# Optimization experiments

Hardware: AMD Instinct MI355X
Metric: run time of the kernel (lower is better)

Reference implementation:

```python
import jax, jax.numpy as jnp
import numpy as np

BN_EPS = 1e-5


def _lin(x, W, b):
    return x @ W.T + b


def reference(input, first_skeleton, noise, first_W, first_b, gru_Wih, gru_Whh,
              gru_bih, gru_bhh, l0_W, l0_b, res_W, res_b, bn_g, bn_b, bn_m, bn_v,
              fl1_W, fl1_b, fl2_W, fl2_b, fl3_W, fl3_b, qkv_W,
              posm_W1, posm_b1, posm_W2, posm_b2, attn_W1, attn_b1, attn_W2, attn_b2):
    B = input.shape[0]
    # first skeleton embedding -> (B, 50, 1)
    sk = _lin(first_skeleton.reshape(B, 36), first_W, first_b).reshape(B, 50, 1)
    # GRU(10 -> 10), batch_first, h0 = 0
    def gru_step(h, x_t):
        gi = x_t @ gru_Wih.T + gru_bih          # (B, 30)
        gh = h @ gru_Whh.T + gru_bhh
        ir, iz, i_n = jnp.split(gi, 3, axis=-1)
        hr, hz, h_n = jnp.split(gh, 3, axis=-1)
        r = jax.nn.sigmoid(ir + hr)
        z = jax.nn.sigmoid(iz + hz)
        n = jnp.tanh(i_n + r * h_n)
        h_new = (1.0 - z) * n + z * h
        return h_new, h_new
    h0 = jnp.zeros((B, 10), input.dtype)
    _, aux = jax.lax.scan(gru_step, h0, jnp.swapaxes(noise, 0, 1))  # (50, B, 10)
    aux = jnp.tanh(jnp.swapaxes(aux, 0, 1))                          # (B, 50, 10)
    x = jnp.concatenate([input, aux, sk], axis=2).reshape(-1, 267)   # (B*50, 267)
    out = _lin(x, l0_W, l0_b)                                        # (B*50, 1024)
    # three residual Linear+BN(eval)+ReLU blocks
    for i in range(3):
        y = out
        for j in range(2):
            y = _lin(y, res_W[i, j], res_b[i, j])
            y = bn_g[i, j] * (y - bn_m[i, j]) * jax.lax.rsqrt(bn_v[i, j] + BN_EPS) + bn_b[i, j]
            y = jax.nn.relu(y)
        out = y + out
    # dropout: eval mode (identity)
    feats = _lin(out, fl1_W, fl1_b).reshape(B, 50, 128)
    pos = _lin(out, fl2_W, fl2_b).reshape(B, 50, 3)
    # PointTransformerLayer (full attention, mask all True -> no-op)
    qkv = feats @ qkv_W.T                                   # (B, 50, 384)
    q, k, v = jnp.split(qkv, 3, axis=-1)
    rel_pos = pos[:, :, None, :] - pos[:, None, :, :]        # (B, 50, 50, 3)
    rel_emb = _lin(jax.nn.relu(_lin(rel_pos, posm_W1, posm_b1)), posm_W2, posm_b2)  # (B,50,50,128)
    qk_rel = q[:, :, None, :] - k[:, None, :, :]             # (B, 50, 50, 128)
    v_ij = v[:, None, :, :] + rel_emb                        # (B, 50, 50, 128)
    sim = _lin(jax.nn.relu(_lin(qk_rel + rel_emb, attn_W1, attn_b1)), attn_W2, attn_b2)
    attn = jax.nn.softmax(sim, axis=-2)                      # softmax over j
    agg = jnp.einsum('bijd,bijd->bid', attn, v_ij)           # (B, 50, 128)
    o = jnp.tanh(_lin(agg, fl3_W, fl3_b))                    # (B, 50, 36)
    return o


def setup_inputs() -> dict:
    key = jax.random.key(0)
    ks = iter(jax.random.split(key, 64))
    def W(*s):
        return jax.random.normal(next(ks), s, jnp.float32) * 0.02
    B = 256
    z = lambda *s: jnp.zeros(s, jnp.float32)
    return {
        'input': jax.random.normal(next(ks), (B, 50, 256), jnp.float32),
        'first_skeleton': jax.random.normal(next(ks), (B, 36), jnp.float32),
        'noise': jax.random.normal(next(ks), (B, 50, 10), jnp.float32) * 0.33,
        'first_W': W(50, 36), 'first_b': z(50),
        'gru_Wih': W(30, 10), 'gru_Whh': W(30, 10), 'gru_bih': z(30), 'gru_bhh': z(30),
        'l0_W': W(1024, 267), 'l0_b': z(1024),
        'res_W': W(3, 2, 1024, 1024), 'res_b': z(3, 2, 1024),
        'bn_g': jnp.ones((3, 2, 1024), jnp.float32), 'bn_b': z(3, 2, 1024),
        'bn_m': z(3, 2, 1024), 'bn_v': jnp.ones((3, 2, 1024), jnp.float32),
        'fl1_W': W(128, 1024), 'fl1_b': z(128),
        'fl2_W': W(3, 1024), 'fl2_b': z(3),
        'fl3_W': W(36, 128), 'fl3_b': z(36),
        'qkv_W': W(384, 128),
        'posm_W1': W(64, 3), 'posm_b1': z(64), 'posm_W2': W(128, 64), 'posm_b2': z(128),
        'attn_W1': W(512, 128), 'attn_b1': z(512), 'attn_W2': W(128, 512), 'attn_b2': z(128),
    }
```

## Files before the change

kernel.cpp:

```cpp
#include <hip/hip_runtime.h>

typedef __attribute__((ext_vector_type(8))) short bf16x8;
typedef __attribute__((ext_vector_type(4))) float f32x4;
typedef __attribute__((ext_vector_type(4))) ushort u16x4;

__device__ __forceinline__ unsigned f2b2(float lo, float hi) {
    unsigned r;
    asm("v_cvt_pk_bf16_f32 %0, %1, %2" : "=v"(r) : "v"(lo), "v"(hi));
    return r;
}
__device__ __forceinline__ ushort f2b(float v) {
    return (ushort)f2b2(v, v);
}
__device__ __forceinline__ float b2f(ushort b) {
    union { float f; unsigned u; } x; x.u = ((unsigned)b) << 16; return x.f;
}

__device__ __forceinline__ void gl_lds16(const void* g, void* l) {
    __builtin_amdgcn_global_load_lds(
        (__attribute__((address_space(1))) void*)(g),
        (__attribute__((address_space(3))) void*)(l), 16, 0, 0);
}


__global__ void k_split(const float* __restrict__ src, ushort* __restrict__ hi,
                        ushort* __restrict__ lo, int rows, int K, int Kpad) {
    long total = (long)rows * Kpad;
    for (long idx = (long)blockIdx.x * 256 + threadIdx.x; idx < total;
         idx += (long)gridDim.x * 256) {
        int r = (int)(idx / Kpad), c = (int)(idx % Kpad);
        float v = (c < K) ? src[(long)r * K + c] : 0.f;
        ushort h = f2b(v);
        hi[idx] = h;
        if (lo) lo[idx] = f2b(v - b2f(h));
    }
}

__global__ void k_wc(const float* __restrict__ qkvW, const float* __restrict__ fl1W,
                     const float* __restrict__ fl1b, float* __restrict__ Wc,
                     float* __restrict__ bc) {
    int idx = blockIdx.x * 256 + threadIdx.x;
    if (idx >= 384 * 1024) return;
    int n = idx >> 10, k = idx & 1023;
    float s = 0.f;
    #pragma unroll 8
    for (int d = 0; d < 128; ++d) s += qkvW[n * 128 + d] * fl1W[d * 1024 + k];
    Wc[idx] = s;
    if (k == 0) {
        float sb = 0.f;
        #pragma unroll 8
        for (int d = 0; d < 128; ++d) sb += qkvW[n * 128 + d] * fl1b[d];
        bc[n] = sb;
    }
}

__global__ void k_sk(const float* __restrict__ fs, const float* __restrict__ fW,
                     const float* __restrict__ fb, float* __restrict__ sk) {
    int m = blockIdx.x * 256 + threadIdx.x;
    if (m >= 12800) return;
    int b = m / 50, i = m % 50;
    float s = fb[i];
    #pragma unroll 4
    for (int c = 0; c < 36; ++c) s += fs[b * 36 + c] * fW[i * 36 + c];
    sk[m] = s;
}

__global__ void k_gru(const float* __restrict__ noise, const float* __restrict__ Wih,
                      const float* __restrict__ Whh, const float* __restrict__ bih,
                      const float* __restrict__ bhh, float* __restrict__ aux) {
    int lane = threadIdx.x & 63;
    int b = blockIdx.x;
    if (b >= 256) return;
    float wih[10] = {}, whh[10] = {};
    float bi = 0.f, bh = 0.f;
    if (lane < 30) {
        #pragma unroll
        for (int c = 0; c < 10; ++c) { wih[c] = Wih[lane * 10 + c]; whh[c] = Whh[lane * 10 + c]; }
        bi = bih[lane]; bh = bhh[lane];
    }
    float h = 0.f;
    for (int t = 0; t < 50; ++t) {
        float xr = (lane < 10) ? noise[(b * 50 + t) * 10 + lane] : 0.f;
        float gi = bi, gh = bh;
        #pragma unroll
        for (int c = 0; c < 10; ++c) {
            float xc = __shfl(xr, c, 64);
            float hc = __shfl(h, c, 64);
            gi += wih[c] * xc; gh += whh[c] * hc;
        }
        float siz = __shfl(gi, lane + 10, 64), shz = __shfl(gh, lane + 10, 64);
        float sin_ = __shfl(gi, lane + 20, 64), shn = __shfl(gh, lane + 20, 64);
        float r = 1.f / (1.f + expf(-(gi + gh)));
        float z = 1.f / (1.f + expf(-(siz + shz)));
        float n = tanhf(sin_ + r * shn);
        float hn = (1.f - z) * n + z * h;
        if (lane < 10) { h = hn; aux[(b * 50 + t) * 10 + lane] = tanhf(hn); }
    }
}

__global__ void k_xbuild(const float* __restrict__ input, const float* __restrict__ aux,
                         const float* __restrict__ sk, ushort* __restrict__ xhi,
                         long M) {
    long idx = (long)blockIdx.x * 256 + threadIdx.x;
    if (idx >= M * 288) return;
    int m = (int)(idx / 288), c = (int)(idx % 288);
    float v;
    if (c < 256) v = input[(long)m * 256 + c];
    else if (c < 266) v = aux[m * 10 + (c - 256)];
    else if (c == 266) v = sk[m];
    else v = 0.f;
    xhi[idx] = f2b(v);
}

template <int MODE>
__global__ __launch_bounds__(256, 3) void k_gemm(
    const ushort* __restrict__ Ahi,
    const ushort* __restrict__ Bhi,
    int N, int K,
    float* outF, ushort* outHi,
    const float* __restrict__ bias,
    const float* __restrict__ bng, const float* __restrict__ bnb,
    const float* __restrict__ bnm, const float* __restrict__ bnv,
    const ushort* resHi) {
    __shared__ __align__(16) ushort S[2][128][32];
    int t = threadIdx.x;
    int flat = blockIdx.y * gridDim.x + blockIdx.x;
    int nwg = gridDim.x * gridDim.y;
    int q = nwg >> 3, r = nwg & 7;
    int xcd = flat & 7, seq = flat >> 3;
    int wgid = (xcd < r ? xcd * (q + 1) : r * (q + 1) + (xcd - r) * q) + seq;
    int bx = wgid % gridDim.x, by = wgid / gridDim.x;
    int m0 = by * 128, n0 = bx * 128;
    int w = t >> 6, lane = t & 63;
    int wm = w >> 1, wn = w & 1;
    int lo16 = lane & 15, hi4 = lane >> 4;

    const int srow = lane >> 2;
    const int skoff = ((lane & 3) ^ (srow & 3)) * 8;
    const int slot8 = (hi4 ^ (lo16 & 3)) * 8;

    f32x4 acc[4][4];
    #pragma unroll
    for (int i = 0; i < 4; ++i)
        #pragma unroll
        for (int j = 0; j < 4; ++j) acc[i][j] = f32x4{0.f, 0.f, 0.f, 0.f};

    const int nk = K / 32;
    for (int kt = 0; kt < nk; ++kt) {
        const int kb = kt * 32;
        #pragma unroll
        for (int i = 0; i < 2; ++i) {
            int rg = w * 32 + i * 16;
            long ga = (long)(m0 + rg + srow) * K + kb + skoff;
            long gb = (long)(n0 + rg + srow) * K + kb + skoff;
            gl_lds16(&Ahi[ga], &S[0][rg][0]);
            gl_lds16(&Bhi[gb], &S[1][rg][0]);
        }
        __syncthreads();
        bf16x8 ah[4], bh[4];
        #pragma unroll
        for (int m = 0; m < 4; ++m) {
            int row = wm * 64 + m * 16 + lo16;
            ah[m] = *(const bf16x8*)&S[0][row][slot8];
        }
        #pragma unroll
        for (int n = 0; n < 4; ++n) {
            int col = wn * 64 + n * 16 + lo16;
            bh[n] = *(const bf16x8*)&S[1][col][slot8];
        }
        #pragma unroll
        for (int m = 0; m < 4; ++m)
            #pragma unroll
            for (int n = 0; n < 4; ++n)
                acc[m][n] = __builtin_amdgcn_mfma_f32_16x16x32_bf16(ah[m], bh[n], acc[m][n], 0, 0, 0);
        __syncthreads();
    }

    #pragma unroll
    for (int n = 0; n < 4; ++n) {
        int gn = n0 + wn * 64 + n * 16 + lo16;
        float bv = bias ? bias[gn] : 0.f;
        float sc = 1.f, sh = 0.f;
        if (MODE >= 1) { sc = bng[gn] * rsqrtf(bnv[gn] + 1e-5f); sh = bnb[gn] - bnm[gn] * sc; }
        #pragma unroll
        for (int m = 0; m < 4; ++m)
            #pragma unroll
            for (int r2 = 0; r2 < 4; ++r2) {
                int gm = m0 + wm * 64 + m * 16 + hi4 * 4 + r2;
                long o = (long)gm * N + gn;
                float v = acc[m][n][r2] + bv;
                if (MODE >= 1) v = fmaxf(v * sc + sh, 0.f);
                if (MODE == 2) v += b2f(resHi[o]);
                if (outF) outF[o] = v;
                if (outHi) outHi[o] = f2b(v);
            }
    }
}

__global__ void k_fl2(const ushort* __restrict__ hA,
                      const float* __restrict__ W, const float* __restrict__ bias,
                      float* __restrict__ pos) {
    int w = threadIdx.x >> 6, lane = threadIdx.x & 63;
    int m = blockIdx.x * 4 + w;
    float a0 = 0.f, a1 = 0.f, a2 = 0.f;
    for (int k0 = lane * 4; k0 < 1024; k0 += 256) {
        long o = (long)m * 1024 + k0;
        u16x4 hv = *(const u16x4*)&hA[o];
        f32x4 w0 = *(const f32x4*)&W[k0];
        f32x4 w1 = *(const f32x4*)&W[1024 + k0];
        f32x4 w2 = *(const f32x4*)&W[2048 + k0];
        #pragma unroll
        for (int e = 0; e < 4; ++e) {
            float x = b2f(hv[e]);
            a0 += x * w0[e]; a1 += x * w1[e]; a2 += x * w2[e];
        }
    }
    #pragma unroll
    for (int off = 32; off; off >>= 1) {
        a0 += __shfl_xor(a0, off, 64);
        a1 += __shfl_xor(a1, off, 64);
        a2 += __shfl_xor(a2, off, 64);
    }
    if (lane == 0) {
        pos[m * 3 + 0] = a0 + bias[0];
        pos[m * 3 + 1] = a1 + bias[1];
        pos[m * 3 + 2] = a2 + bias[2];
    }
}

__global__ __launch_bounds__(256, 3) void k_attn2(
    const float* __restrict__ qkv, const float* __restrict__ posb,
    const ushort* __restrict__ W1b, const ushort* __restrict__ W2b,
    const float* __restrict__ b1, const ushort* __restrict__ pW2b,
    const float* __restrict__ pW1, const float* __restrict__ pb1,
    const float* __restrict__ pb2,
    const float* __restrict__ fl3W, const float* __restrict__ fl3b,
    float* __restrict__ out, long mbase) {
    __shared__ __align__(16) char smem[49152];
    int flat = blockIdx.x, nwg = gridDim.x;
    int q = nwg >> 3, r = nwg & 7;
    int xcd = flat & 7, seq = flat >> 3;
    int wgid = (xcd < r ? xcd * (q + 1) : r * (q + 1) + (xcd - r) * q) + seq;
    int bi0 = wgid * 2;
    int t = threadIdx.x, w = t >> 6, lane = t & 63;
    int lo16 = lane & 15, hi4 = lane >> 4;
    char* H1 = smem + 32768;

    {
        int rl = t & 127, eh = t >> 7;
        int biL = bi0 + (rl >> 6);
        int j = rl & 63; int jc = j < 50 ? j : 49;
        int bL = biL / 50;
        int kv = bL * 50 + jc;
        float d0 = posb[biL * 3] - posb[kv * 3];
        float d1 = posb[biL * 3 + 1] - posb[kv * 3 + 1];
        float d2 = posb[biL * 3 + 2] - posb[kv * 3 + 2];
        int swm = (rl & 7) << 4;
        #pragma unroll
        for (int e0 = 0; e0 < 32; e0 += 2) {
            int e = eh * 32 + e0;
            float v0 = fmaxf(pb1[e] + pW1[e * 3] * d0 + pW1[e * 3 + 1] * d1
                             + pW1[e * 3 + 2] * d2, 0.f);
            float v1 = fmaxf(pb1[e + 1] + pW1[e * 3 + 3] * d0 + pW1[e * 3 + 4] * d1
                             + pW1[e * 3 + 5] * d2, 0.f);
            *(unsigned*)(H1 + rl * 128 + ((e * 2) ^ swm)) = f2b2(v0, v1);
        }
    }
    __syncthreads();

    {
        f32x4 racc[8][2];
        #pragma unroll
        for (int m = 0; m < 8; ++m)
            #pragma unroll
            for (int n = 0; n < 2; ++n) racc[m][n] = f32x4{0.f, 0.f, 0.f, 0.f};
        #pragma unroll
        for (int kt = 0; kt < 2; ++kt) {
            int k0 = kt * 32 + hi4 * 8;
            bf16x8 bv[2];
            #pragma unroll
            for (int n = 0; n < 2; ++n)
                bv[n] = *(const bf16x8*)&pW2b[(w * 32 + n * 16 + lo16) * 64 + k0];
            #pragma unroll
            for (int m = 0; m < 8; ++m) {
                int row = m * 16 + lo16;
                bf16x8 ha = *(const bf16x8*)(H1 + row * 128 + ((k0 * 2) ^ ((lo16 & 7) << 4)));
                #pragma unroll
                for (int n = 0; n < 2; ++n)
                    racc[m][n] = __builtin_amdgcn_mfma_f32_16x16x32_bf16(ha, bv[n], racc[m][n], 0, 0, 0);
            }
        }
        #pragma unroll
        for (int m = 0; m < 8; ++m)
            #pragma unroll
            for (int n = 0; n < 2; ++n) {
                int col = w * 32 + n * 16 + lo16;
                float pb = pb2[col];
                #pragma unroll
                for (int rr = 0; rr < 4; ++rr) {
                    int row = m * 16 + hi4 * 4 + rr;
                    *(ushort*)(smem + row * 256 + ((col * 2) ^ ((row & 15) << 4))) =
                        f2b(racc[m][n][rr] + pb);
                }
            }
    }
    __syncthreads();

    #pragma unroll
    for (int cc = 0; cc < 8; ++cc) {
        int c = cc * 256 + t;
        int row = c >> 4, g16 = c & 15;
        int biL = bi0 + (row >> 6);
        int j = row & 63;
        char* addr = smem + row * 256 + ((g16 * 16) ^ ((row & 15) << 4));
        bf16x8 tv;
        if (j < 50) {
            int bL = biL / 50;
            long kq = (long)biL * 384 + g16 * 8;
            long kk = (long)(bL * 50 + j) * 384 + 128 + g16 * 8;
            f32x4 q0 = *(const f32x4*)&qkv[kq];
            f32x4 q1 = *(const f32x4*)&qkv[kq + 4];
            f32x4 k0v = *(const f32x4*)&qkv[kk];
            f32x4 k1v = *(const f32x4*)&qkv[kk + 4];
            bf16x8 rv = *(bf16x8*)addr;
            unsigned* tu = (unsigned*)&tv;
            #pragma unroll
            for (int i = 0; i < 2; ++i)
                tu[i] = f2b2(q0[2 * i] - k0v[2 * i] + b2f((ushort)rv[2 * i]),
                             q0[2 * i + 1] - k0v[2 * i + 1] + b2f((ushort)rv[2 * i + 1]));
            #pragma unroll
            for (int i = 0; i < 2; ++i)
                tu[2 + i] = f2b2(q1[2 * i] - k1v[2 * i] + b2f((ushort)rv[4 + 2 * i]),
                                 q1[2 * i + 1] - k1v[2 * i + 1] + b2f((ushort)rv[4 + 2 * i + 1]));
        } else {
            #pragma unroll
            for (int e = 0; e < 8; ++e) tv[e] = 0;
        }
        *(bf16x8*)addr = tv;
    }
    __syncthreads();

    f32x4 acc2[8][2];
    #pragma unroll
    for (int m = 0; m < 8; ++m)
        #pragma unroll
        for (int n = 0; n < 2; ++n) acc2[m][n] = f32x4{0.f, 0.f, 0.f, 0.f};

    for (int e8 = 0; e8 < 8; ++e8) {
        f32x4 acc1[8];
        #pragma unroll
        for (int m = 0; m < 8; ++m) acc1[m] = f32x4{0.f, 0.f, 0.f, 0.f};
        __builtin_amdgcn_s_setprio(1);
        #pragma unroll
        for (int kt = 0; kt < 4; ++kt) {
            int col = e8 * 64 + w * 16 + lo16;
            int k0 = kt * 32 + hi4 * 8;
            bf16x8 bfv = *(const bf16x8*)&W1b[(long)col * 128 + k0];
            #pragma unroll
            for (int m = 0; m < 8; ++m) {
                int row = m * 16 + lo16;
                bf16x8 af = *(const bf16x8*)(smem + row * 256 +
                              ((k0 * 2) ^ ((row & 15) << 4)));
                acc1[m] = __builtin_amdgcn_mfma_f32_16x16x32_bf16(af, bfv, acc1[m], 0, 0, 0);
            }
        }
        __builtin_amdgcn_s_setprio(0);
        __syncthreads();
        {
            int ch = w * 16 + lo16;
            float bb = b1[e8 * 64 + ch];
            #pragma unroll
            for (int m = 0; m < 8; ++m) {
                unsigned p01 = f2b2(fmaxf(acc1[m][0] + bb, 0.f), fmaxf(acc1[m][1] + bb, 0.f));
                unsigned p23 = f2b2(fmaxf(acc1[m][2] + bb, 0.f), fmaxf(acc1[m][3] + bb, 0.f));
                int r0 = m * 16 + hi4 * 4;
                *(ushort*)(H1 + (r0 + 0) * 128 + ((ch * 2) ^ (((r0 + 0) & 7) << 4))) = (ushort)p01;
                *(ushort*)(H1 + (r0 + 1) * 128 + ((ch * 2) ^ (((r0 + 1) & 7) << 4))) = (ushort)(p01 >> 16);
                *(ushort*)(H1 + (r0 + 2) * 128 + ((ch * 2) ^ (((r0 + 2) & 7) << 4))) = (ushort)p23;
                *(ushort*)(H1 + (r0 + 3) * 128 + ((ch * 2) ^ (((r0 + 3) & 7) << 4))) = (ushort)(p23 >> 16);
            }
        }
        __syncthreads();
        #pragma unroll
        for (int kt2 = 0; kt2 < 2; ++kt2) {
            int k0 = kt2 * 32 + hi4 * 8;
            bf16x8 af2[8];
            #pragma unroll
            for (int m = 0; m < 8; ++m) {
                int row = m * 16 + lo16;
                af2[m] = *(const bf16x8*)(H1 + row * 128 + ((k0 * 2) ^ ((lo16 & 7) << 4)));
            }
            __builtin_amdgcn_s_setprio(1);
            #pragma unroll
            for (int n = 0; n < 2; ++n) {
                int col = w * 32 + n * 16 + lo16;
                bf16x8 w2 = *(const bf16x8*)&W2b[(long)col * 512 + e8 * 64 + k0];
                #pragma unroll
                for (int m = 0; m < 8; ++m)
                    acc2[m][n] = __builtin_amdgcn_mfma_f32_16x16x32_bf16(af2[m], w2, acc2[m][n], 0, 0, 0);
            }
            __builtin_amdgcn_s_setprio(0);
        }
    }
    __syncthreads();

    {
        int rl = t & 127, eh = t >> 7;
        int biL = bi0 + (rl >> 6);
        int j = rl & 63; int jc = j < 50 ? j : 49;
        int bL = biL / 50;
        int kv = bL * 50 + jc;
        float d0 = posb[biL * 3] - posb[kv * 3];
        float d1 = posb[biL * 3 + 1] - posb[kv * 3 + 1];
        float d2 = posb[biL * 3 + 2] - posb[kv * 3 + 2];
        int swm = (rl & 7) << 4;
        #pragma unroll
        for (int e0 = 0; e0 < 32; e0 += 2) {
            int e = eh * 32 + e0;
            float v0 = fmaxf(pb1[e] + pW1[e * 3] * d0 + pW1[e * 3 + 1] * d1
                             + pW1[e * 3 + 2] * d2, 0.f);
            float v1 = fmaxf(pb1[e + 1] + pW1[e * 3 + 3] * d0 + pW1[e * 3 + 4] * d1
                             + pW1[e * 3 + 5] * d2, 0.f);
            *(unsigned*)(H1 + rl * 128 + ((e * 2) ^ swm)) = f2b2(v0, v1);
        }
    }
    __syncthreads();

    #pragma unroll 1
    for (int mh = 0; mh < 2; ++mh) {
        f32x4 racc[4][2];
        #pragma unroll
        for (int m = 0; m < 4; ++m)
            #pragma unroll
            for (int n = 0; n < 2; ++n) racc[m][n] = f32x4{0.f, 0.f, 0.f, 0.f};
        #pragma unroll
        for (int kt = 0; kt < 2; ++kt) {
            int k0 = kt * 32 + hi4 * 8;
            bf16x8 bv[2];
            #pragma unroll
            for (int n = 0; n < 2; ++n)
                bv[n] = *(const bf16x8*)&pW2b[(w * 32 + n * 16 + lo16) * 64 + k0];
            #pragma unroll
            for (int m = 0; m < 4; ++m) {
                int row = (mh * 4 + m) * 16 + lo16;
                bf16x8 ha = *(const bf16x8*)(H1 + row * 128 + ((k0 * 2) ^ ((lo16 & 7) << 4)));
                #pragma unroll
                for (int n = 0; n < 2; ++n)
                    racc[m][n] = __builtin_amdgcn_mfma_f32_16x16x32_bf16(ha, bv[n], racc[m][n], 0, 0, 0);
            }
        }
        #pragma unroll
        for (int m = 0; m < 4; ++m)
            #pragma unroll
            for (int n = 0; n < 2; ++n) {
                int col = w * 32 + n * 16 + lo16;
                float pb = pb2[col];
                #pragma unroll
                for (int rr = 0; rr < 4; ++rr) {
                    int row = (mh * 4 + m) * 16 + hi4 * 4 + rr;
                    *(ushort*)(smem + row * 256 + ((col * 2) ^ ((row & 15) << 4))) =
                        f2b(racc[m][n][rr] + pb);
                }
            }
    }
    __syncthreads();

    float* aggF = (float*)H1;
    float* part = (float*)(H1 + 1024);
    #pragma unroll
    for (int bs = 0; bs < 2; ++bs) {
        int biL = bi0 + bs;
        int bL = biL / 50;
        float outv[2];
        #pragma unroll
        for (int n = 0; n < 2; ++n) {
            float mx = -1e30f;
            #pragma unroll
            for (int m = 0; m < 4; ++m)
                #pragma unroll
                for (int rr = 0; rr < 4; ++rr) {
                    int j = m * 16 + hi4 * 4 + rr;
                    if (j < 50) mx = fmaxf(mx, acc2[bs * 4 + m][n][rr]);
                }
            mx = fmaxf(mx, __shfl_xor(mx, 16, 64));
            mx = fmaxf(mx, __shfl_xor(mx, 32, 64));
            float e[4][4];
            float sum = 0.f;
            #pragma unroll
            for (int m = 0; m < 4; ++m)
                #pragma unroll
                for (int rr = 0; rr < 4; ++rr) {
                    int j = m * 16 + hi4 * 4 + rr;
                    float ev = (j < 50) ? __expf(acc2[bs * 4 + m][n][rr] - mx) : 0.f;
                    e[m][rr] = ev; sum += ev;
                }
            sum += __shfl_xor(sum, 16, 64);
            sum += __shfl_xor(sum, 32, 64);
            float inv = 1.f / sum;
            int col = w * 32 + n * 16 + lo16;
            float ag = 0.f;
            #pragma unroll
            for (int m = 0; m < 4; ++m)
                #pragma unroll
                for (int rr = 0; rr < 4; ++rr) {
                    int j = m * 16 + hi4 * 4 + rr;
                    if (j < 50) {
                        int row = bs * 64 + j;
                        float rl = b2f(*(const ushort*)(smem + row * 256 +
                                      ((col * 2) ^ ((j & 15) << 4))));
                        float vv = qkv[(long)(bL * 50 + j) * 384 + 256 + col] + rl;
                        ag += e[m][rr] * inv * vv;
                    }
                }
            ag += __shfl_xor(ag, 16, 64);
            ag += __shfl_xor(ag, 32, 64);
            outv[n] = ag;
        }
        if (hi4 == 0) {
            aggF[bs * 128 + w * 32 + lo16] = outv[0];
            aggF[bs * 128 + w * 32 + 16 + lo16] = outv[1];
        }
        if (lane < 36) {
            const float* wf = &fl3W[lane * 128 + w * 32];
            const float* af = aggF + bs * 128 + w * 32;
            float s = 0.f;
            #pragma unroll 8
            for (int d = 0; d < 32; ++d) s += af[d] * wf[d];
            part[bs * 144 + w * 36 + lane] = s;
        }
    }
    __syncthreads();

    if (t < 36) {
        float s = fl3b[t] + part[t] + part[36 + t] + part[72 + t] + part[108 + t];
        out[(mbase + bi0) * 36 + t] = tanhf(s);
    } else if (t >= 128 && t < 164) {
        int tt = t - 128;
        float s = fl3b[tt] + part[144 + tt] + part[144 + 36 + tt]
                + part[144 + 72 + tt] + part[144 + 108 + tt];
        out[(mbase + bi0 + 1) * 36 + tt] = tanhf(s);
    }
}

struct Bufs {
    float *sk, *aux, *qkvF, *posb, *WcF, *bc;
    ushort *xh, *actAh, *actBh;
    ushort *l0Wh, *resWh, *Wch, *aW1b, *aW2b, *pW2b;
};

static size_t plan_ws(char* ws, long MCr, Bufs& B) {
    size_t off = 0;
    auto alloc = [&](size_t n) { char* p = ws + off; off += (n + 255) & ~(size_t)255; return p; };
    B.sk    = (float*) alloc(12800L * 4);
    B.aux   = (float*) alloc(128000L * 4);
    B.xh    = (ushort*)alloc((size_t)MCr * 288 * 2);
    B.actAh = (ushort*)alloc((size_t)MCr * 1024 * 2);
    B.actBh = (ushort*)alloc((size_t)MCr * 1024 * 2);
    B.qkvF  = (float*) alloc((size_t)MCr * 384 * 4);
    B.posb  = (float*) alloc((size_t)MCr * 3 * 4);
    B.l0Wh  = (ushort*)alloc(1024L * 288 * 2);
    B.resWh = (ushort*)alloc(6144L * 1024 * 2);
    B.WcF   = (float*) alloc(384L * 1024 * 4);
    B.Wch   = (ushort*)alloc(384L * 1024 * 2);
    B.bc    = (float*) alloc(384L * 4);
    B.aW1b  = (ushort*)alloc(512L * 128 * 2);
    B.aW2b  = (ushort*)alloc(128L * 512 * 2);
    B.pW2b  = (ushort*)alloc(128L * 64 * 2);
    return off;
}

extern "C" void kernel_launch(void* const* d_in, const int* in_sizes, int n_in,
                              void* d_out, int out_size, void* d_ws, size_t ws_size,
                              hipStream_t stream) {
    (void)in_sizes; (void)n_in;
    const float* input  = (const float*)d_in[0];
    const float* fskel  = (const float*)d_in[1];
    const float* noise  = (const float*)d_in[2];
    const float* firstW = (const float*)d_in[3];
    const float* firstB = (const float*)d_in[4];
    const float* gWih   = (const float*)d_in[5];
    const float* gWhh   = (const float*)d_in[6];
    const float* gbih   = (const float*)d_in[7];
    const float* gbhh   = (const float*)d_in[8];
    const float* l0W    = (const float*)d_in[9];
    const float* l0b    = (const float*)d_in[10];
    const float* resW   = (const float*)d_in[11];
    const float* resB   = (const float*)d_in[12];
    const float* bnG    = (const float*)d_in[13];
    const float* bnB    = (const float*)d_in[14];
    const float* bnM    = (const float*)d_in[15];
    const float* bnV    = (const float*)d_in[16];
    const float* fl1W   = (const float*)d_in[17];
    const float* fl1b   = (const float*)d_in[18];
    const float* fl2W   = (const float*)d_in[19];
    const float* fl2b   = (const float*)d_in[20];
    const float* fl3W   = (const float*)d_in[21];
    const float* fl3b   = (const float*)d_in[22];
    const float* qkvW   = (const float*)d_in[23];
    const float* pW1    = (const float*)d_in[24];
    const float* pb1    = (const float*)d_in[25];
    const float* pW2    = (const float*)d_in[26];
    const float* pb2    = (const float*)d_in[27];
    const float* aW1    = (const float*)d_in[28];
    const float* ab1    = (const float*)d_in[29];
    const float* aW2    = (const float*)d_in[30];
    float* out = (float*)d_out;

    char* ws = (char*)d_ws;
    Bufs B;
    long MCr = 12800;
    while (plan_ws(ws, MCr, B) > ws_size) {
        MCr >>= 1;
        if (MCr < 1600) {
            hipMemsetAsync(d_out, 0, (size_t)out_size * sizeof(float), stream);
            return;
        }
    }
    const int nchunks = (int)(12800 / MCr);

    k_split<<<1152, 256, 0, stream>>>(l0W, B.l0Wh, nullptr, 1024, 267, 288);
    k_split<<<8192, 256, 0, stream>>>(resW, B.resWh, nullptr, 6144, 1024, 1024);
    k_wc<<<1536, 256, 0, stream>>>(qkvW, fl1W, fl1b, B.WcF, B.bc);
    k_split<<<1536, 256, 0, stream>>>(B.WcF, B.Wch, nullptr, 384, 1024, 1024);
    k_split<<<256, 256, 0, stream>>>(aW1, B.aW1b, nullptr, 512, 128, 128);
    k_split<<<256, 256, 0, stream>>>(aW2, B.aW2b, nullptr, 128, 512, 512);
    k_split<<<32, 256, 0, stream>>>(pW2, B.pW2b, nullptr, 128, 64, 64);
    k_sk<<<50, 256, 0, stream>>>(fskel, firstW, firstB, B.sk);
    k_gru<<<256, 64, 0, stream>>>(noise, gWih, gWhh, gbih, gbhh, B.aux);

    for (int c = 0; c < nchunks; ++c) {
        long mbase = (long)c * MCr;
        int xb_grid = (int)((MCr * 288 + 255) / 256);
        k_xbuild<<<xb_grid, 256, 0, stream>>>(input + mbase * 256, B.aux + mbase * 10,
                                              B.sk + mbase, B.xh, MCr);
        dim3 gt(8, (unsigned)(MCr / 128));
        k_gemm<0><<<gt, 256, 0, stream>>>(B.xh, B.l0Wh, 1024, 288,
            nullptr, B.actAh, l0b, nullptr, nullptr, nullptr, nullptr, nullptr);
        for (int blk = 0; blk < 3; ++blk) {
            int j0 = blk * 2, j1 = blk * 2 + 1;
            k_gemm<1><<<gt, 256, 0, stream>>>(B.actAh,
                B.resWh + (size_t)j0 * 1024 * 1024,
                1024, 1024, nullptr, B.actBh, resB + j0 * 1024,
                bnG + j0 * 1024, bnB + j0 * 1024, bnM + j0 * 1024, bnV + j0 * 1024,
                nullptr);
            k_gemm<2><<<gt, 256, 0, stream>>>(B.actBh,
                B.resWh + (size_t)j1 * 1024 * 1024,
                1024, 1024, nullptr, B.actAh, resB + j1 * 1024,
                bnG + j1 * 1024, bnB + j1 * 1024, bnM + j1 * 1024, bnV + j1 * 1024,
                B.actAh);
        }
        dim3 gq(3, (unsigned)(MCr / 128));
        k_gemm<0><<<gq, 256, 0, stream>>>(B.actAh, B.Wch, 384, 1024,
            B.qkvF, nullptr, B.bc, nullptr, nullptr, nullptr, nullptr, nullptr);
        k_fl2<<<(int)(MCr / 4), 256, 0, stream>>>(B.actAh, fl2W, fl2b, B.posb);
        k_attn2<<<(int)(MCr / 2), 256, 0, stream>>>(B.qkvF, B.posb, B.aW1b, B.aW2b,
                                                    ab1, B.pW2b, pW1, pb1, pb2,
                                                    fl3W, fl3b, out, mbase);
    }
}
```

Before: 1.063 ms.

## Process attention rows one at a time, spilling second row's logits to LDS in fp16

The second query row's attention logits (acc2[4..7]) are packed to fp16 and parked in shared memory. The rel-pos embedding and softmax/aggregation then run in a loop over the two rows, one at a time. This roughly halves the live accumulator registers in the epilogue and the LDS footprint for the rel-pos MLP, which could allow more occupancy. In exchange it adds an extra barrier per row, serialises the two rows, and reduces the second row's logits to fp16 precision.

```diff
diff --git a/kernel.cpp b/kernel.cpp
--- a/kernel.cpp
+++ b/kernel.cpp
@@ -14,6 +14,14 @@
 }
 __device__ __forceinline__ float b2f(ushort b) {
     union { float f; unsigned u; } x; x.u = ((unsigned)b) << 16; return x.f;
+}
+__device__ __forceinline__ unsigned pkf16(float a, float b) {
+    unsigned r;
+    asm("v_cvt_pkrtz_f16_f32 %0, %1, %2" : "=v"(r) : "v"(a), "v"(b));
+    return r;
+}
+__device__ __forceinline__ float h2f(ushort s) {
+    union { ushort s; _Float16 h; } x; x.s = s; return (float)x.h;
 }
 
 __device__ __forceinline__ void gl_lds16(const void* g, void* l) {
@@ -405,72 +413,101 @@
     __syncthreads();
 
     {
-        int rl = t & 127, eh = t >> 7;
-        int biL = bi0 + (rl >> 6);
-        int j = rl & 63; int jc = j < 50 ? j : 49;
-        int bL = biL / 50;
-        int kv = bL * 50 + jc;
-        float d0 = posb[biL * 3] - posb[kv * 3];
-        float d1 = posb[biL * 3 + 1] - posb[kv * 3 + 1];
-        float d2 = posb[biL * 3 + 2] - posb[kv * 3 + 2];
-        int swm = (rl & 7) << 4;
-        #pragma unroll
-        for (int e0 = 0; e0 < 32; e0 += 2) {
-            int e = eh * 32 + e0;
-            float v0 = fmaxf(pb1[e] + pW1[e * 3] * d0 + pW1[e * 3 + 1] * d1
-                             + pW1[e * 3 + 2] * d2, 0.f);
-            float v1 = fmaxf(pb1[e + 1] + pW1[e * 3 + 3] * d0 + pW1[e * 3 + 4] * d1
-                             + pW1[e * 3 + 5] * d2, 0.f);
-            *(unsigned*)(H1 + rl * 128 + ((e * 2) ^ swm)) = f2b2(v0, v1);
-        }
-    }
-    __syncthreads();
+        unsigned* P = (unsigned*)H1;
+        #pragma unroll
+        for (int m = 0; m < 4; ++m)
+            #pragma unroll
+            for (int n = 0; n < 2; ++n) {
+                P[((m * 2 + n) * 2 + 0) * 256 + t] = pkf16(acc2[4 + m][n][0], acc2[4 + m][n][1]);
+                P[((m * 2 + n) * 2 + 1) * 256 + t] = pkf16(acc2[4 + m][n][2], acc2[4 + m][n][3]);
+            }
+    }
+
+    float* aggF = (float*)(smem + 24576);
+    float* part = (float*)(smem + 25088);
 
     #pragma unroll 1
-    for (int mh = 0; mh < 2; ++mh) {
-        f32x4 racc[4][2];
-        #pragma unroll
-        for (int m = 0; m < 4; ++m)
-            #pragma unroll
-            for (int n = 0; n < 2; ++n) racc[m][n] = f32x4{0.f, 0.f, 0.f, 0.f};
-        #pragma unroll
-        for (int kt = 0; kt < 2; ++kt) {
-            int k0 = kt * 32 + hi4 * 8;
-            bf16x8 bv[2];
-            #pragma unroll
-            for (int n = 0; n < 2; ++n)
-                bv[n] = *(const bf16x8*)&pW2b[(w * 32 + n * 16 + lo16) * 64 + k0];
-            #pragma unroll
-            for (int m = 0; m < 4; ++m) {
-                int row = (mh * 4 + m) * 16 + lo16;
-                bf16x8 ha = *(const bf16x8*)(H1 + row * 128 + ((k0 * 2) ^ ((lo16 & 7) << 4)));
-                #pragma unroll
-                for (int n = 0; n < 2; ++n)
-                    racc[m][n] = __builtin_amdgcn_mfma_f32_16x16x32_bf16(ha, bv[n], racc[m][n], 0, 0, 0);
-            }
-        }
-        #pragma unroll
-        for (int m = 0; m < 4; ++m)
-            #pragma unroll
-            for (int n = 0; n < 2; ++n) {
-                int col = w * 32 + n * 16 + lo16;
-                float pb = pb2[col];
-                #pragma unroll
-                for (int rr = 0; rr < 4; ++rr) {
-                    int row = (mh * 4 + m) * 16 + hi4 * 4 + rr;
-                    *(ushort*)(smem + row * 256 + ((col * 2) ^ ((row & 15) << 4))) =
-                        f2b(racc[m][n][rr] + pb);
-                }
-            }
-    }
-    __syncthreads();
-
-    float* aggF = (float*)H1;
-    float* part = (float*)(H1 + 1024);
-    #pragma unroll
     for (int bs = 0; bs < 2; ++bs) {
         int biL = bi0 + bs;
         int bL = biL / 50;
+        f32x4 cur[4][2];
+        if (bs == 0) {
+            #pragma unroll
+            for (int m = 0; m < 4; ++m)
+                #pragma unroll
+                for (int n = 0; n < 2; ++n) cur[m][n] = acc2[m][n];
+        } else {
+            const unsigned* P = (const unsigned*)H1;
+            #pragma unroll
+            for (int m = 0; m < 4; ++m)
+                #pragma unroll
+                for (int n = 0; n < 2; ++n) {
+                    unsigned u0 = P[((m * 2 + n) * 2 + 0) * 256 + t];
+                    unsigned u1 = P[((m * 2 + n) * 2 + 1) * 256 + t];
+                    cur[m][n][0] = h2f((ushort)u0);
+                    cur[m][n][1] = h2f((ushort)(u0 >> 16));
+                    cur[m][n][2] = h2f((ushort)u1);
+                    cur[m][n][3] = h2f((ushort)(u1 >> 16));
+                }
+        }
+        {
+            int rl = t & 63, eq = t >> 6;
+            int jc = rl < 50 ? rl : 49;
+            int kv = bL * 50 + jc;
+            float d0 = posb[biL * 3] - posb[kv * 3];
+            float d1 = posb[biL * 3 + 1] - posb[kv * 3 + 1];
+            float d2 = posb[biL * 3 + 2] - posb[kv * 3 + 2];
+            int swm = (rl & 7) << 4;
+            #pragma unroll
+            for (int e0 = 0; e0 < 16; e0 += 2) {
+                int e = eq * 16 + e0;
+                float v0 = fmaxf(pb1[e] + pW1[e * 3] * d0 + pW1[e * 3 + 1] * d1
+                                 + pW1[e * 3 + 2] * d2, 0.f);
+                float v1 = fmaxf(pb1[e + 1] + pW1[e * 3 + 3] * d0 + pW1[e * 3 + 4] * d1
+                                 + pW1[e * 3 + 5] * d2, 0.f);
+                *(unsigned*)(smem + rl * 128 + ((e * 2) ^ swm)) = f2b2(v0, v1);
+            }
+        }
+        __syncthreads();
+        {
+            f32x4 racc[4][2];
+            #pragma unroll
+            for (int m = 0; m < 4; ++m)
+                #pragma unroll
+                for (int n = 0; n < 2; ++n) racc[m][n] = f32x4{0.f, 0.f, 0.f, 0.f};
+            #pragma unroll
+            for (int kt = 0; kt < 2; ++kt) {
+                int k0 = kt * 32 + hi4 * 8;
+                bf16x8 bv[2];
+                #pragma unroll
+                for (int n = 0; n < 2; ++n)
+                    bv[n] = *(const bf16x8*)&pW2b[(w * 32 + n * 16 + lo16) * 64 + k0];
+                #pragma unroll
+                for (int m = 0; m < 4; ++m) {
+                    int row = m * 16 + lo16;
+                    bf16x8 ha = *(const bf16x8*)(smem + row * 128 +
+                                  ((k0 * 2) ^ ((lo16 & 7) << 4)));
+                    #pragma unroll
+                    for (int n = 0; n < 2; ++n)
+                        racc[m][n] = __builtin_amdgcn_mfma_f32_16x16x32_bf16(ha, bv[n], racc[m][n], 0, 0, 0);
+                }
+            }
+            #pragma unroll
+            for (int m = 0; m < 4; ++m)
+                #pragma unroll
+                for (int n = 0; n < 2; ++n) {
+                    int col = w * 32 + n * 16 + lo16;
+                    float pb = pb2[col];
+                    #pragma unroll
+                    for (int rr = 0; rr < 4; ++rr) {
+                        int row = m * 16 + hi4 * 4 + rr;
+                        *(ushort*)(smem + 8192 + row * 256 +
+                                   ((col * 2) ^ ((row & 15) << 4))) =
+                            f2b(racc[m][n][rr] + pb);
+                    }
+                }
+        }
+
         float outv[2];
         #pragma unroll
         for (int n = 0; n < 2; ++n) {
@@ -480,7 +517,7 @@
                 #pragma unroll
                 for (int rr = 0; rr < 4; ++rr) {
                     int j = m * 16 + hi4 * 4 + rr;
-                    if (j < 50) mx = fmaxf(mx, acc2[bs * 4 + m][n][rr]);
+                    if (j < 50) mx = fmaxf(mx, cur[m][n][rr]);
                 }
             mx = fmaxf(mx, __shfl_xor(mx, 16, 64));
             mx = fmaxf(mx, __shfl_xor(mx, 32, 64));
@@ -491,7 +528,7 @@
                 #pragma unroll
                 for (int rr = 0; rr < 4; ++rr) {
                     int j = m * 16 + hi4 * 4 + rr;
-                    float ev = (j < 50) ? __expf(acc2[bs * 4 + m][n][rr] - mx) : 0.f;
+                    float ev = (j < 50) ? __expf(cur[m][n][rr] - mx) : 0.f;
                     e[m][rr] = ev; sum += ev;
                 }
             sum += __shfl_xor(sum, 16, 64);
@@ -505,8 +542,7 @@
                 for (int rr = 0; rr < 4; ++rr) {
                     int j = m * 16 + hi4 * 4 + rr;
                     if (j < 50) {
-                        int row = bs * 64 + j;
-                        float rl = b2f(*(const ushort*)(smem + row * 256 +
+                        float rl = b2f(*(const ushort*)(smem + 8192 + j * 256 +
                                       ((col * 2) ^ ((j & 15) << 4))));
                         float vv = qkv[(long)(bL * 50 + j) * 384 + 256 + col] + rl;
                         ag += e[m][rr] * inv * vv;
@@ -517,19 +553,19 @@
             outv[n] = ag;
         }
         if (hi4 == 0) {
-            aggF[bs * 128 + w * 32 + lo16] = outv[0];
-            aggF[bs * 128 + w * 32 + 16 + lo16] = outv[1];
+            aggF[w * 32 + lo16] = outv[0];
+            aggF[w * 32 + 16 + lo16] = outv[1];
         }
         if (lane < 36) {
             const float* wf = &fl3W[lane * 128 + w * 32];
-            const float* af = aggF + bs * 128 + w * 32;
+            const float* af = aggF + w * 32;
             float s = 0.f;
             #pragma unroll 8
             for (int d = 0; d < 32; ++d) s += af[d] * wf[d];
             part[bs * 144 + w * 36 + lane] = s;
         }
-    }
-    __syncthreads();
+        __syncthreads();
+    }
 
     if (t < 36) {
         float s = fl3b[t] + part[t] + part[36 + t] + part[72 + t] + part[108 + t];
```

Measured after the change: 1.128 ms. +6.1%, slower.
